# Kernel optimization log

Hardware: AMD Instinct MI355X
Metric: run time of the kernel (lower is better)

## Reference

```python
import jax, jax.numpy as jnp
import numpy as np

B, IC, H, W = 32, 128, 112, 112
OC, K, STRIDE, PAD = 256, 3, 2, 1


def setup_inputs() -> dict:
    key = jax.random.key(0)
    kx, kw = jax.random.split(key)
    x = jax.random.normal(kx, (B, IC, H, W), dtype=jnp.float32)
    weight = jax.random.normal(kw, (OC, IC, K, K), dtype=jnp.float32) * 0.01
    bias = jnp.zeros((OC,), dtype=jnp.float32)
    return {"x": x, "weight": weight, "bias": bias}


def reference(x, weight, bias):
    # Equivalent of the nested-loop conv: standard cross-correlation,
    # stride=2, zero padding=1, NCHW / OIHW layouts.
    out = jax.lax.conv_general_dilated(
        x, weight,
        window_strides=(STRIDE, STRIDE),
        padding=[(PAD, PAD), (PAD, PAD)],
        dimension_numbers=("NCHW", "OIHW", "NCHW"),
    )
    return out + bias[None, :, None, None]
```

## Files before the change

kernel.cpp:

```cpp
#include <hip/hip_runtime.h>
#include <hip/hip_bf16.h>


#define B_    32
#define IC_   128
#define H_    112
#define W_    112
#define HW_   (H_ * W_)
#define OC_   256
#define OH_   56
#define OW_   56
#define HP    113
#define NPIX  (B_ * OH_ * OW_)
#define XT_BYTES ((size_t)B_ * HP * HP * IC_ * 2)
#define WT_BYTES ((size_t)9 * OC_ * IC_ * 2)

typedef __attribute__((ext_vector_type(8))) short bf16x8;
typedef __attribute__((ext_vector_type(4))) float f32x4;

static __device__ __forceinline__ unsigned f2bf_u(float f) {
  union { float f; unsigned u; } v; v.f = f;
  return (v.u + 0x7FFF + ((v.u >> 16) & 1)) >> 16;
}

static __device__ __forceinline__ unsigned pk_bf16(float a, float b) {
  union { __hip_bfloat162 h; unsigned u; } c;
  c.h = __float22bfloat162_rn(float2{a, b});
  return c.u;
}

__global__ __launch_bounds__(256) void xtrans_kernel(
    const float* __restrict__ x, unsigned short* __restrict__ xt) {
  __shared__ unsigned short lds[128 * 128];
  const int ihp = blockIdx.x;
  const int b   = blockIdx.y;
  const int tid = threadIdx.x;

  if (ihp > 0) {
    const float* xp = x + (size_t)b * IC_ * HW_ + (size_t)(ihp - 1) * W_;
#pragma unroll
    for (int it = 0; it < 14; ++it) {
      const int i  = tid + it * 256;
      const int ic = i / 28;
      const int g  = i - ic * 28;
      const float4 v = *reinterpret_cast<const float4*>(
          xp + (size_t)ic * HW_ + g * 4);
      uint2 p;
      p.x = pk_bf16(v.x, v.y);
      p.y = pk_bf16(v.z, v.w);
      const int gs = g ^ ((ic >> 3) & 7);
      *reinterpret_cast<uint2*>(&lds[ic * 128 + gs * 4]) = p;
    }
  }
  __syncthreads();

  unsigned short* xrow = xt + ((size_t)(b * HP + ihp)) * (HP * IC_);
  const bool live = (ihp > 0);
#pragma unroll
  for (int it = 0; it < 8; ++it) {
    const int e = tid + it * 256;
    if (e >= HP * 16) break;
    const int iwp = e >> 4;
    const int icg = e & 15;
    uint4 v = {0u, 0u, 0u, 0u};
    if (live && iwp > 0) {
      const int iw  = iwp - 1;
      const int col = ((iw >> 2) ^ (icg & 7)) * 4 + (iw & 3);
      const int r0  = icg * 8;
      unsigned u0 = lds[(r0 + 0) * 128 + col];
      unsigned u1 = lds[(r0 + 1) * 128 + col];
      unsigned u2 = lds[(r0 + 2) * 128 + col];
      unsigned u3 = lds[(r0 + 3) * 128 + col];
      unsigned u4 = lds[(r0 + 4) * 128 + col];
      unsigned u5 = lds[(r0 + 5) * 128 + col];
      unsigned u6 = lds[(r0 + 6) * 128 + col];
      unsigned u7 = lds[(r0 + 7) * 128 + col];
      v.x = u0 | (u1 << 16);
      v.y = u2 | (u3 << 16);
      v.z = u4 | (u5 << 16);
      v.w = u6 | (u7 << 16);
    }
    *reinterpret_cast<uint4*>(xrow + iwp * IC_ + icg * 8) = v;
  }
}

__global__ __launch_bounds__(256) void wtrans_kernel(
    const float* __restrict__ w, unsigned short* __restrict__ wt) {
  const int t  = blockIdx.x * 256 + threadIdx.x;
  const int oc = t >> 7;
  const int ic = t & 127;
  const float* ws = w + (size_t)t * 9;
#pragma unroll
  for (int tap = 0; tap < 9; ++tap)
    wt[((size_t)tap * OC_ + oc) * IC_ + ic] = (unsigned short)f2bf_u(ws[tap]);
}

__global__ __launch_bounds__(256) void conv_mfma_kernel(
    const unsigned short* __restrict__ xt, const unsigned short* __restrict__ wt,
    const float* __restrict__ bias, float* __restrict__ out) {
  __shared__ short Ws[2][128 * 32];
  __shared__ short Xs[2][128 * 32];

  const int tid  = threadIdx.x;
  const int wav  = tid >> 6;
  const int lane = tid & 63;

  const int bid  = blockIdx.x;
  const int wgid = (bid & 7) * 196 + (bid >> 3);
  const int mt  = wgid & 1;
  const int pt  = wgid >> 1;
  const int oc0 = mt * 128;
  const int p0  = pt * 128;

  const int l2 = lane >> 2;
  const int lc = lane & 3;
  const char* xsrc[2];
  const char* wsrc[2];
#pragma unroll
  for (int i = 0; i < 2; ++i) {
    const int pix = p0 + wav * 32 + i * 16 + l2;
    const int b   = pix / 3136;
    const int q   = pix - b * 3136;
    const int oh  = q / 56;
    const int ow  = q - oh * 56;
    const size_t e = (((size_t)b * HP + 2 * oh) * HP + 2 * ow) * IC_;
    xsrc[i] = reinterpret_cast<const char*>(xt) + e * 2 + lc * 16;
    const int ocr = oc0 + wav * 32 + i * 16 + l2;
    wsrc[i] = reinterpret_cast<const char*>(wt) + (size_t)ocr * IC_ * 2 + lc * 16;
  }
  char* xdst = reinterpret_cast<char*>(&Xs[0][0]) + wav * 2048;
  char* wdst = reinterpret_cast<char*>(&Ws[0][0]) + wav * 2048;

  const int wm  = wav >> 1;
  const int wn  = wav & 1;
  const int l15 = lane & 15;
  const int kg  = (lane >> 4) * 8;
  const short* wrow = &Ws[0][0] + ((wm * 64 + l15) * 32 + kg);
  const short* xrow = &Xs[0][0] + ((wn * 64 + l15) * 32 + kg);

  f32x4 acc[4][4] = {};

  auto stage = [&](int buf, int tap, int icc) {
    const int kh = tap / 3;
    const int kw = tap - kh * 3;
    const size_t xoff = ((size_t)(kh * HP + kw) * IC_ + icc * 32) * 2;
    const size_t woff = ((size_t)tap * OC_ * IC_ + icc * 32) * 2;
    char* xd = xdst + buf * (128 * 32 * 2);
    char* wd = wdst + buf * (128 * 32 * 2);
#pragma unroll
    for (int i = 0; i < 2; ++i) {
      __builtin_amdgcn_global_load_lds(
          (const __attribute__((address_space(1))) void*)(xsrc[i] + xoff),
          (__attribute__((address_space(3))) void*)(xd + i * 1024), 16, 0, 0);
      __builtin_amdgcn_global_load_lds(
          (const __attribute__((address_space(1))) void*)(wsrc[i] + woff),
          (__attribute__((address_space(3))) void*)(wd + i * 1024), 16, 0, 0);
    }
  };

  auto compute = [&](int buf) {
    const short* wr = wrow + buf * (128 * 32);
    const short* xr = xrow + buf * (128 * 32);
    bf16x8 af[4], bfr[4];
#pragma unroll
    for (int mi = 0; mi < 4; ++mi)
      af[mi] = *reinterpret_cast<const bf16x8*>(wr + mi * 16 * 32);
#pragma unroll
    for (int ni = 0; ni < 4; ++ni)
      bfr[ni] = *reinterpret_cast<const bf16x8*>(xr + ni * 16 * 32);
#pragma unroll
    for (int mi = 0; mi < 4; ++mi)
#pragma unroll
      for (int ni = 0; ni < 4; ++ni)
        acc[mi][ni] = __builtin_amdgcn_mfma_f32_16x16x32_bf16(
            af[mi], bfr[ni], acc[mi][ni], 0, 0, 0);
  };

  stage(0, 0, 0);
  __syncthreads();

  for (int tap = 0; tap < 9; ++tap) {
    const bool lt = (tap == 8);
    stage(1, tap, 1);  compute(0);  __syncthreads();
    stage(0, tap, 2);  compute(1);  __syncthreads();
    stage(1, tap, 3);  compute(0);  __syncthreads();
    if (!lt) { stage(0, tap + 1, 0); }
    compute(1);
    if (!lt) { __syncthreads(); }
  }

#pragma unroll
  for (int mi = 0; mi < 4; ++mi) {
#pragma unroll
    for (int j = 0; j < 4; ++j) {
      const int oc = oc0 + wm * 64 + mi * 16 + (lane >> 4) * 4 + j;
      const float bv = bias[oc];
#pragma unroll
      for (int ni = 0; ni < 4; ++ni) {
        const int pix = p0 + wn * 64 + ni * 16 + l15;
        const int b   = pix / 3136;
        const int q   = pix - b * 3136;
        out[((size_t)b * OC_ + oc) * 3136 + q] = acc[mi][ni][j] + bv;
      }
    }
  }
}

__global__ __launch_bounds__(256) void conv2d_f32_kernel(
    const float* __restrict__ x, const float* __restrict__ w,
    const float* __restrict__ bias, float* __restrict__ out) {
  __shared__ float wlds[IC_ * 9][8];
  const int b   = blockIdx.z;
  const int oc0 = blockIdx.y * 8;
  const float* wsrc = w + (size_t)oc0 * (IC_ * 9);
  for (int i = threadIdx.x; i < IC_ * 9 * 8; i += 256) {
    const int j = i / (IC_ * 9);
    const int t = i - j * (IC_ * 9);
    wlds[t][j] = wsrc[(size_t)j * (IC_ * 9) + t];
  }
  __syncthreads();
  const int p  = blockIdx.x * 256 + threadIdx.x;
  const int ow = p % OW_;
  const int oh = p / OW_;
  const bool pv = (oh < OH_);
  const int ih0 = 2 * oh - 1;
  const int iw0 = 2 * ow - 1;
  const float* xb = x + (size_t)b * IC_ * HW_ + (ptrdiff_t)ih0 * W_ + iw0;
  float acc[8];
#pragma unroll
  for (int j = 0; j < 8; ++j) acc[j] = 0.f;
  for (int ic = 0; ic < IC_; ++ic) {
    const float* xc = xb + (size_t)ic * HW_;
#pragma unroll
    for (int kh = 0; kh < 3; ++kh) {
      const bool hv = pv && ((ih0 + kh) >= 0);
#pragma unroll
      for (int kw = 0; kw < 3; ++kw) {
        const bool v = hv && ((iw0 + kw) >= 0);
        const float xv = v ? xc[kh * W_ + kw] : 0.f;
        const int t = ic * 9 + kh * 3 + kw;
        const float4 w0 = *reinterpret_cast<const float4*>(&wlds[t][0]);
        const float4 w1 = *reinterpret_cast<const float4*>(&wlds[t][4]);
        acc[0] = fmaf(xv, w0.x, acc[0]); acc[1] = fmaf(xv, w0.y, acc[1]);
        acc[2] = fmaf(xv, w0.z, acc[2]); acc[3] = fmaf(xv, w0.w, acc[3]);
        acc[4] = fmaf(xv, w1.x, acc[4]); acc[5] = fmaf(xv, w1.y, acc[5]);
        acc[6] = fmaf(xv, w1.z, acc[6]); acc[7] = fmaf(xv, w1.w, acc[7]);
      }
    }
  }
  if (pv) {
#pragma unroll
    for (int j = 0; j < 8; ++j)
      out[(((size_t)(b * OC_ + oc0 + j)) * OH_ + oh) * OW_ + ow] =
          acc[j] + bias[oc0 + j];
  }
}

extern "C" void kernel_launch(void* const* d_in, const int* in_sizes, int n_in,
                              void* d_out, int out_size, void* d_ws, size_t ws_size,
                              hipStream_t stream) {
  const float* x    = (const float*)d_in[0];
  const float* w    = (const float*)d_in[1];
  const float* bias = (const float*)d_in[2];
  float* out        = (float*)d_out;

  if (ws_size >= XT_BYTES + WT_BYTES) {
    unsigned short* xt  = (unsigned short*)d_ws;
    unsigned short* wtp = (unsigned short*)((char*)d_ws + XT_BYTES);
    xtrans_kernel<<<dim3(HP, B_), 256, 0, stream>>>(x, xt);
    wtrans_kernel<<<128, 256, 0, stream>>>(w, wtp);
    conv_mfma_kernel<<<(NPIX / 128) * 2, 256, 0, stream>>>(xt, wtp, bias, out);
  } else {
    conv2d_f32_kernel<<<dim3(13, OC_ / 8, B_), 256, 0, stream>>>(x, w, bias, out);
  }
}
```

Measured before the change: 157.4 us.

## Deepen conv K-loop pipeline to four LDS buffers with partial vmcnt waits

Replaces the double-buffered K loop with a 4-slot LDS ring that keeps three stages of async global-to-LDS loads in flight. Each stage now waits with a partial s_waitcnt vmcnt and a raw s_barrier fenced by sched_barrier, instead of a full __syncthreads. The aim is to hide global load latency behind MFMA work and cut barrier stalls. The cost is doubling LDS per block to 64KB, which can lower the number of resident workgroups per CU.

```diff
diff --git a/kernel.cpp b/kernel.cpp
--- a/kernel.cpp
+++ b/kernel.cpp
@@ -98,8 +98,8 @@
 __global__ __launch_bounds__(256) void conv_mfma_kernel(
     const unsigned short* __restrict__ xt, const unsigned short* __restrict__ wt,
     const float* __restrict__ bias, float* __restrict__ out) {
-  __shared__ short Ws[2][128 * 32];
-  __shared__ short Xs[2][128 * 32];
+  __shared__ short Ws[4][128 * 32];
+  __shared__ short Xs[4][128 * 32];
 
   const int tid  = threadIdx.x;
   const int wav  = tid >> 6;
@@ -140,13 +140,15 @@
 
   f32x4 acc[4][4] = {};
 
-  auto stage = [&](int buf, int tap, int icc) {
+  auto stage = [&](int s, int buf) {
+    const int tap = s >> 2;
+    const int icc = s & 3;
     const int kh = tap / 3;
     const int kw = tap - kh * 3;
     const size_t xoff = ((size_t)(kh * HP + kw) * IC_ + icc * 32) * 2;
     const size_t woff = ((size_t)tap * OC_ * IC_ + icc * 32) * 2;
-    char* xd = xdst + buf * (128 * 32 * 2);
-    char* wd = wdst + buf * (128 * 32 * 2);
+    char* xd = xdst + buf * 8192;
+    char* wd = wdst + buf * 8192;
 #pragma unroll
     for (int i = 0; i < 2; ++i) {
       __builtin_amdgcn_global_load_lds(
@@ -176,18 +178,31 @@
             af[mi], bfr[ni], acc[mi][ni], 0, 0, 0);
   };
 
-  stage(0, 0, 0);
-  __syncthreads();
-
-  for (int tap = 0; tap < 9; ++tap) {
-    const bool lt = (tap == 8);
-    stage(1, tap, 1);  compute(0);  __syncthreads();
-    stage(0, tap, 2);  compute(1);  __syncthreads();
-    stage(1, tap, 3);  compute(0);  __syncthreads();
-    if (!lt) { stage(0, tap + 1, 0); }
-    compute(1);
-    if (!lt) { __syncthreads(); }
-  }
+#define FENCED_BARRIER()                          \
+  __builtin_amdgcn_sched_barrier(0);              \
+  __builtin_amdgcn_s_barrier();                   \
+  __builtin_amdgcn_sched_barrier(0)
+
+  stage(0, 0);
+  stage(1, 1);
+  stage(2, 2);
+
+  for (int s = 0; s < 33; ++s) {
+    asm volatile("s_waitcnt vmcnt(8)" ::: "memory");
+    FENCED_BARRIER();
+    stage(s + 3, (s + 3) & 3);
+    compute(s & 3);
+  }
+  asm volatile("s_waitcnt vmcnt(8)" ::: "memory");
+  FENCED_BARRIER();
+  compute(33 & 3);
+  asm volatile("s_waitcnt vmcnt(4)" ::: "memory");
+  FENCED_BARRIER();
+  compute(34 & 3);
+  asm volatile("s_waitcnt vmcnt(0)" ::: "memory");
+  FENCED_BARRIER();
+  compute(35 & 3);
+#undef FENCED_BARRIER
 
 #pragma unroll
   for (int mi = 0; mi < 4; ++mi) {
```

Measured after the change: 175.6 us. 1.12x slower.
